# Performance work log

Measured on AMD Instinct MI355X. Metric: run time of the kernel, lower is better.

## Reference

```python
import jax, jax.numpy as jnp
import numpy as np

B, IN_SIZE, P = 16384, 4096, 8
D = IN_SIZE // P  # 512


def setup_inputs() -> dict:
    key = jax.random.key(0)
    ks = jax.random.split(key, 10)
    bound = 1.0 / np.sqrt(D)  # fan_in = int_dim
    return {
        "x": jax.random.normal(ks[0], (B, IN_SIZE), dtype=jnp.float32),
        "weights1": jax.random.uniform(ks[1], (P, D, D), jnp.float32, -bound, bound),
        "bias1": jax.random.uniform(ks[2], (IN_SIZE,), jnp.float32, -bound, bound),
        "weights2": jax.random.uniform(ks[3], (P, D, D), jnp.float32, -bound, bound),
        "bias2": jax.random.uniform(ks[4], (IN_SIZE,), jnp.float32, -bound, bound),
        # trainable swish params (init 0 as in torch code)
        "gamma1": jnp.zeros((IN_SIZE,), jnp.float32),
        "beta1": jnp.zeros((IN_SIZE,), jnp.float32),
        "gamma3": jnp.zeros((IN_SIZE,), jnp.float32),
        "beta3": jnp.zeros((IN_SIZE,), jnp.float32),
        # Affine norms (scalar gain/bias)
        "gain1": jnp.ones((1,), jnp.float32),
        "nbias1": jnp.zeros((1,), jnp.float32),
        "gain3": jnp.ones((1,), jnp.float32),
        "nbias3": jnp.zeros((1,), jnp.float32),
    }


def _swish(x, gamma, beta):
    # f(x) = (gamma + sigmoid(beta*x) * (1-gamma)) * x
    return (gamma + jax.nn.sigmoid(beta * x) * (1.0 - gamma)) * x


def _block_matmul(x, w):
    # x: [B, IN_SIZE] -> [B, P, D]; block-diagonal matmul == batched per-partition GEMM
    xb = x.reshape(x.shape[0], P, D)
    return jnp.einsum("bpd,pde->bpe", xb, w).reshape(x.shape[0], IN_SIZE)


def reference(x, weights1, bias1, weights2, bias2, gamma1, beta1, gamma3, beta3,
              gain1, nbias1, gain3, nbias3):
    o1 = _swish(_block_matmul(x * gain1 + nbias1, weights1) + bias1, gamma1, beta1)
    o2 = _swish(_block_matmul(o1 * gain3 + nbias3, weights2) + bias2, gamma3, beta3) + x
    return o2
```

## Files before the change

### kernel.cpp

```cpp
#include <hip/hip_runtime.h>
#include <cstdint>
#include <cstddef>


#define B_ROWS 16384
#define IN_SZ  4096
#define P_PART 8
#define D_DIM  512
#define M_BLK  64

typedef unsigned short ushort_t;
typedef __attribute__((ext_vector_type(8))) short short8;
typedef __attribute__((ext_vector_type(4))) float f32x4;

__device__ inline unsigned short f2bf(float f) {
  union { float f; unsigned int u; } c; c.f = f;
  unsigned int u = c.u;
  return (unsigned short)((u + 0x7fffu + ((u >> 16) & 1u)) >> 16);
}

__device__ inline int swz(int m, int c) { return m * D_DIM + (c ^ ((m & 7) << 3)); }

__global__ __launch_bounds__(256) void wconv_kernel(const float* __restrict__ w1,
                                                    const float* __restrict__ w2,
                                                    ushort_t* __restrict__ wt1,
                                                    ushort_t* __restrict__ wt2) {
  __shared__ float tile[64][68];
  const int p = blockIdx.z & 7;
  const float*  src = (blockIdx.z < 8) ? w1 : w2;
  ushort_t*     dst = (blockIdx.z < 8) ? wt1 : wt2;
  const int k0 = blockIdx.x * 64;
  const int n0 = blockIdx.y * 64;
  const int t = threadIdx.x;

  const float* base = src + ((size_t)p * D_DIM + k0) * D_DIM + n0;
#pragma unroll
  for (int i = 0; i < 4; ++i) {
    int f = t + i * 256;
    int kr = f >> 4;
    int c4 = f & 15;
    float4 v = *(const float4*)(base + (size_t)kr * D_DIM + c4 * 4);
    *(float4*)(&tile[kr][c4 * 4]) = v;
  }
  __syncthreads();
  ushort_t* obase = dst + ((size_t)p * D_DIM + n0) * D_DIM + k0;
#pragma unroll
  for (int i = 0; i < 4; ++i) {
    int f = t + i * 256;
    int nr = f >> 4;
    int kc = (f & 15) * 4;
    unsigned int lo = f2bf(tile[kc + 0][nr]) | ((unsigned int)f2bf(tile[kc + 1][nr]) << 16);
    unsigned int hi = f2bf(tile[kc + 2][nr]) | ((unsigned int)f2bf(tile[kc + 3][nr]) << 16);
    uint2 pk; pk.x = lo; pk.y = hi;
    *(uint2*)(obase + (size_t)nr * D_DIM + kc) = pk;
  }
}

__global__ __launch_bounds__(512, 4) void fused_kernel(
    const float* __restrict__ x,
    const ushort_t* __restrict__ wt1, const ushort_t* __restrict__ wt2,
    const float* __restrict__ bias1, const float* __restrict__ gamma1,
    const float* __restrict__ beta1,
    const float* __restrict__ bias2, const float* __restrict__ gamma3,
    const float* __restrict__ beta3,
    const float* __restrict__ gain1, const float* __restrict__ nbias1,
    const float* __restrict__ gain3, const float* __restrict__ nbias3,
    float* __restrict__ out) {
  __shared__ __align__(16) ushort_t Xs[M_BLK * D_DIM];

  const int t = threadIdx.x;
  const int lane = t & 63, wn = t >> 6;
  const int l15 = lane & 15, quad = lane >> 4;
  const int p  = blockIdx.x;
  const int m0 = blockIdx.y * M_BLK;

  const float g1 = gain1[0], nb1 = nbias1[0];
  const float g3 = gain3[0], nb3 = nbias3[0];

  {
    const float* xb = x + (size_t)m0 * IN_SZ + (size_t)p * D_DIM;
#pragma unroll
    for (int i = 0; i < 16; ++i) {
      int g = t + i * 512;
      int m = g >> 7;
      int c = (g & 127) * 4;
      float4 v = *(const float4*)(xb + (size_t)m * IN_SZ + c);
      uint2 pk;
      pk.x = f2bf(v.x * g1 + nb1) | ((unsigned int)f2bf(v.y * g1 + nb1) << 16);
      pk.y = f2bf(v.z * g1 + nb1) | ((unsigned int)f2bf(v.w * g1 + nb1) << 16);
      *(uint2*)(&Xs[swz(m, c)]) = pk;
    }
  }
  __syncthreads();

  f32x4 acc[4][4];
#pragma unroll
  for (int i = 0; i < 4; ++i)
#pragma unroll
    for (int j = 0; j < 4; ++j) acc[i][j] = (f32x4)(0.0f);

  {
    const ushort_t* w1b = wt1 + (size_t)p * D_DIM * D_DIM
                              + (size_t)(wn * 64 + l15) * D_DIM;
#pragma unroll 2
    for (int kt = 0; kt < 8; ++kt) {
#pragma unroll
      for (int kk = 0; kk < 2; ++kk) {
        const int kof = kt * 64 + kk * 32 + quad * 8;
        short8 a[4], b[4];
#pragma unroll
        for (int i = 0; i < 4; ++i)
          a[i] = *(const short8*)(w1b + (size_t)(i * 16) * D_DIM + kof);
#pragma unroll
        for (int j = 0; j < 4; ++j)
          b[j] = *(const short8*)(&Xs[swz(j * 16 + l15, kof)]);
#pragma unroll
        for (int i = 0; i < 4; ++i)
#pragma unroll
          for (int j = 0; j < 4; ++j)
            acc[i][j] = __builtin_amdgcn_mfma_f32_16x16x32_bf16(a[i], b[j], acc[i][j], 0, 0, 0);
      }
    }
  }

  __syncthreads();

#pragma unroll
  for (int i = 0; i < 4; ++i) {
    const int n = wn * 64 + i * 16 + quad * 4;
    const int col = p * D_DIM + n;
    const float4 bv = *(const float4*)(bias1 + col);
    const float4 ga = *(const float4*)(gamma1 + col);
    const float4 be = *(const float4*)(beta1 + col);
#pragma unroll
    for (int j = 0; j < 4; ++j) {
      const int m = j * 16 + l15;
      float o[4];
#pragma unroll
      for (int r = 0; r < 4; ++r) {
        float v = acc[i][j][r] + ((const float*)&bv)[r];
        float g = ((const float*)&ga)[r];
        float sg = 1.0f / (1.0f + __expf(-((const float*)&be)[r] * v));
        o[r] = ((g + sg * (1.0f - g)) * v) * g3 + nb3;
      }
      uint2 pk;
      pk.x = f2bf(o[0]) | ((unsigned int)f2bf(o[1]) << 16);
      pk.y = f2bf(o[2]) | ((unsigned int)f2bf(o[3]) << 16);
      *(uint2*)(&Xs[swz(m, n)]) = pk;
    }
  }
  __syncthreads();

  f32x4 acc2[4][4];
#pragma unroll
  for (int i = 0; i < 4; ++i)
#pragma unroll
    for (int j = 0; j < 4; ++j) acc2[i][j] = (f32x4)(0.0f);

  {
    const ushort_t* w2b = wt2 + (size_t)p * D_DIM * D_DIM
                              + (size_t)(wn * 64 + l15) * D_DIM;
#pragma unroll 2
    for (int kt = 0; kt < 8; ++kt) {
#pragma unroll
      for (int kk = 0; kk < 2; ++kk) {
        const int kof = kt * 64 + kk * 32 + quad * 8;
        short8 a[4], b[4];
#pragma unroll
        for (int i = 0; i < 4; ++i)
          a[i] = *(const short8*)(&Xs[swz(i * 16 + l15, kof)]);
#pragma unroll
        for (int j = 0; j < 4; ++j)
          b[j] = *(const short8*)(w2b + (size_t)(j * 16) * D_DIM + kof);
#pragma unroll
        for (int i = 0; i < 4; ++i)
#pragma unroll
          for (int j = 0; j < 4; ++j)
            acc2[i][j] = __builtin_amdgcn_mfma_f32_16x16x32_bf16(a[i], b[j], acc2[i][j], 0, 0, 0);
      }
    }
  }

  const int colg0 = p * D_DIM + wn * 64;
#pragma unroll
  for (int j = 0; j < 4; ++j) {
    const int col = colg0 + j * 16 + l15;
    const float bv = bias2[col], ga = gamma3[col], be = beta3[col];
#pragma unroll
    for (int i = 0; i < 4; ++i) {
      const int r0 = m0 + i * 16 + quad * 4;
#pragma unroll
      for (int r = 0; r < 4; ++r) {
        float v = acc2[i][j][r] + bv;
        float sg = 1.0f / (1.0f + __expf(-be * v));
        float o = (ga + sg * (1.0f - ga)) * v;
        const size_t idx = (size_t)(r0 + r) * IN_SZ + col;
        out[idx] = o + x[idx];
      }
    }
  }
}

extern "C" void kernel_launch(void* const* d_in, const int* in_sizes, int n_in,
                              void* d_out, int out_size, void* d_ws, size_t ws_size,
                              hipStream_t stream) {
  const float* x      = (const float*)d_in[0];
  const float* w1     = (const float*)d_in[1];
  const float* b1     = (const float*)d_in[2];
  const float* w2     = (const float*)d_in[3];
  const float* b2     = (const float*)d_in[4];
  const float* gamma1 = (const float*)d_in[5];
  const float* beta1  = (const float*)d_in[6];
  const float* gamma3 = (const float*)d_in[7];
  const float* beta3  = (const float*)d_in[8];
  const float* gain1  = (const float*)d_in[9];
  const float* nbias1 = (const float*)d_in[10];
  const float* gain3  = (const float*)d_in[11];
  const float* nbias3 = (const float*)d_in[12];
  float* out = (float*)d_out;

  ushort_t* wt1 = (ushort_t*)d_ws;
  ushort_t* wt2 = wt1 + (size_t)P_PART * D_DIM * D_DIM;

  wconv_kernel<<<dim3(8, 8, 16), 256, 0, stream>>>(w1, w2, wt1, wt2);
  fused_kernel<<<dim3(P_PART, B_ROWS / M_BLK), 512, 0, stream>>>(
      x, wt1, wt2, b1, gamma1, beta1, b2, gamma3, beta3,
      gain1, nbias1, gain3, nbias3, out);
}
```

Baseline: 749.9 us.

## Stream weight tiles through LDS with async global_load_lds double buffering

Both GEMM phases now load weight fragments into a per-wave double-buffered LDS region using direct global-to-LDS loads, issued two k-steps ahead. Explicit vmcnt/lgkmcnt waits, a sched_barrier and MFMA priority raising overlap the weight fetch with the matrix math, replacing direct global register loads. LDS use grows by 64KB per block and the occupancy hint drops from 4 to 2 blocks per CU, which may reduce latency hiding across waves. The hand-placed waitcnts also make correctness depend on the exact order in which loads are issued.

```diff
diff --git a/kernel.cpp b/kernel.cpp
--- a/kernel.cpp
+++ b/kernel.cpp
@@ -17,6 +17,12 @@
   union { float f; unsigned int u; } c; c.f = f;
   unsigned int u = c.u;
   return (unsigned short)((u + 0x7fffu + ((u >> 16) & 1u)) >> 16);
+}
+
+__device__ inline void gld_to_lds16(const void* g, void* l) {
+  __builtin_amdgcn_global_load_lds((const __attribute__((address_space(1))) void*)g,
+                                   (__attribute__((address_space(3))) void*)l,
+                                   16, 0, 0);
 }
 
 __device__ inline int swz(int m, int c) { return m * D_DIM + (c ^ ((m & 7) << 3)); }
@@ -56,7 +62,7 @@
   }
 }
 
-__global__ __launch_bounds__(512, 4) void fused_kernel(
+__global__ __launch_bounds__(512, 2) void fused_kernel(
     const float* __restrict__ x,
     const ushort_t* __restrict__ wt1, const ushort_t* __restrict__ wt2,
     const float* __restrict__ bias1, const float* __restrict__ gamma1,
@@ -67,6 +73,7 @@
     const float* __restrict__ gain3, const float* __restrict__ nbias3,
     float* __restrict__ out) {
   __shared__ __align__(16) ushort_t Xs[M_BLK * D_DIM];
+  __shared__ __align__(16) ushort_t Ws[8 * 4096];
 
   const int t = threadIdx.x;
   const int lane = t & 63, wn = t >> 6;
@@ -76,6 +83,21 @@
 
   const float g1 = gain1[0], nb1 = nbias1[0];
   const float g3 = gain3[0], nb3 = nbias3[0];
+
+  const ushort_t* w1r = wt1 + (size_t)p * D_DIM * D_DIM + (size_t)(wn * 64 + l15) * D_DIM;
+  const ushort_t* w2r = wt2 + (size_t)p * D_DIM * D_DIM + (size_t)(wn * 64 + l15) * D_DIM;
+  ushort_t* pb = Ws + wn * 4096;
+
+#define STAGE_W(wr, s, buf) do {                                               \
+    const ushort_t* g_ = (wr) + (s) * 32 + quad * 8;                           \
+    gld_to_lds16(g_,                         pb + (buf) * 2048);               \
+    gld_to_lds16(g_ + (size_t)16 * D_DIM,    pb + (buf) * 2048 + 512);         \
+    gld_to_lds16(g_ + (size_t)32 * D_DIM,    pb + (buf) * 2048 + 1024);        \
+    gld_to_lds16(g_ + (size_t)48 * D_DIM,    pb + (buf) * 2048 + 1536);        \
+  } while (0)
+
+  STAGE_W(w1r, 0, 0);
+  STAGE_W(w1r, 1, 1);
 
   {
     const float* xb = x + (size_t)m0 * IN_SZ + (size_t)p * D_DIM;
@@ -99,31 +121,35 @@
 #pragma unroll
     for (int j = 0; j < 4; ++j) acc[i][j] = (f32x4)(0.0f);
 
-  {
-    const ushort_t* w1b = wt1 + (size_t)p * D_DIM * D_DIM
-                              + (size_t)(wn * 64 + l15) * D_DIM;
-#pragma unroll 2
-    for (int kt = 0; kt < 8; ++kt) {
-#pragma unroll
-      for (int kk = 0; kk < 2; ++kk) {
-        const int kof = kt * 64 + kk * 32 + quad * 8;
-        short8 a[4], b[4];
-#pragma unroll
-        for (int i = 0; i < 4; ++i)
-          a[i] = *(const short8*)(w1b + (size_t)(i * 16) * D_DIM + kof);
-#pragma unroll
-        for (int j = 0; j < 4; ++j)
-          b[j] = *(const short8*)(&Xs[swz(j * 16 + l15, kof)]);
-#pragma unroll
-        for (int i = 0; i < 4; ++i)
-#pragma unroll
-          for (int j = 0; j < 4; ++j)
-            acc[i][j] = __builtin_amdgcn_mfma_f32_16x16x32_bf16(a[i], b[j], acc[i][j], 0, 0, 0);
-      }
-    }
-  }
-
-  __syncthreads();
+#pragma unroll
+  for (int s = 0; s < 16; ++s) {
+    if (s < 15) asm volatile("s_waitcnt vmcnt(4)" ::: "memory");
+    else        asm volatile("s_waitcnt vmcnt(0)" ::: "memory");
+    const ushort_t* pc = pb + (s & 1) * 2048;
+    short8 a[4], b[4];
+#pragma unroll
+    for (int i = 0; i < 4; ++i)
+      a[i] = *(const short8*)(pc + i * 512 + lane * 8);
+    const int kof = s * 32 + quad * 8;
+#pragma unroll
+    for (int j = 0; j < 4; ++j)
+      b[j] = *(const short8*)(&Xs[swz(j * 16 + l15, kof)]);
+    asm volatile("s_waitcnt lgkmcnt(0)" ::: "memory");
+    __builtin_amdgcn_sched_barrier(0);
+    if (s + 2 < 16) STAGE_W(w1r, s + 2, s & 1);
+    __builtin_amdgcn_s_setprio(1);
+#pragma unroll
+    for (int i = 0; i < 4; ++i)
+#pragma unroll
+      for (int j = 0; j < 4; ++j)
+        acc[i][j] = __builtin_amdgcn_mfma_f32_16x16x32_bf16(a[i], b[j], acc[i][j], 0, 0, 0);
+    __builtin_amdgcn_s_setprio(0);
+  }
+
+  __syncthreads();
+
+  STAGE_W(w2r, 0, 0);
+  STAGE_W(w2r, 1, 1);
 
 #pragma unroll
   for (int i = 0; i < 4; ++i) {
@@ -157,28 +183,29 @@
 #pragma unroll
     for (int j = 0; j < 4; ++j) acc2[i][j] = (f32x4)(0.0f);
 
-  {
-    const ushort_t* w2b = wt2 + (size_t)p * D_DIM * D_DIM
-                              + (size_t)(wn * 64 + l15) * D_DIM;
-#pragma unroll 2
-    for (int kt = 0; kt < 8; ++kt) {
-#pragma unroll
-      for (int kk = 0; kk < 2; ++kk) {
-        const int kof = kt * 64 + kk * 32 + quad * 8;
-        short8 a[4], b[4];
-#pragma unroll
-        for (int i = 0; i < 4; ++i)
-          a[i] = *(const short8*)(&Xs[swz(i * 16 + l15, kof)]);
-#pragma unroll
-        for (int j = 0; j < 4; ++j)
-          b[j] = *(const short8*)(w2b + (size_t)(j * 16) * D_DIM + kof);
-#pragma unroll
-        for (int i = 0; i < 4; ++i)
-#pragma unroll
-          for (int j = 0; j < 4; ++j)
-            acc2[i][j] = __builtin_amdgcn_mfma_f32_16x16x32_bf16(a[i], b[j], acc2[i][j], 0, 0, 0);
-      }
-    }
+#pragma unroll
+  for (int s = 0; s < 16; ++s) {
+    if (s < 15) asm volatile("s_waitcnt vmcnt(4)" ::: "memory");
+    else        asm volatile("s_waitcnt vmcnt(0)" ::: "memory");
+    const ushort_t* pc = pb + (s & 1) * 2048;
+    short8 a[4], b[4];
+    const int kof = s * 32 + quad * 8;
+#pragma unroll
+    for (int i = 0; i < 4; ++i)
+      a[i] = *(const short8*)(&Xs[swz(i * 16 + l15, kof)]);
+#pragma unroll
+    for (int j = 0; j < 4; ++j)
+      b[j] = *(const short8*)(pc + j * 512 + lane * 8);
+    asm volatile("s_waitcnt lgkmcnt(0)" ::: "memory");
+    __builtin_amdgcn_sched_barrier(0);
+    if (s + 2 < 16) STAGE_W(w2r, s + 2, s & 1);
+    __builtin_amdgcn_s_setprio(1);
+#pragma unroll
+    for (int i = 0; i < 4; ++i)
+#pragma unroll
+      for (int j = 0; j < 4; ++j)
+        acc2[i][j] = __builtin_amdgcn_mfma_f32_16x16x32_bf16(a[i], b[j], acc2[i][j], 0, 0, 0);
+    __builtin_amdgcn_s_setprio(0);
   }
 
   const int colg0 = p * D_DIM + wn * 64;
@@ -199,6 +226,7 @@
       }
     }
   }
+#undef STAGE_W
 }
 
 extern "C" void kernel_launch(void* const* d_in, const int* in_sizes, int n_in,
```

Result: slower. 770.0 us (+2.7%).
